# Optimization experiments

Measured on AMD Instinct MI355X. Metric: run time of the kernel, lower is better.

Reference implementation:

```python
import jax, jax.numpy as jnp
import numpy as np

EPS = 1e-6
N_HEADS = 128
QK_NOPE = 128
QK_ROPE = 64
KV_RANK = 512

def rmsnorm(x, gamma):
    var = jnp.mean(jnp.square(x), axis=-1, keepdims=True)
    return x * jax.lax.rsqrt(var + EPS) * gamma

def apply_rope(x, cos, sin):
    # x: [..., D], cos/sin broadcastable to x; rotate-half convention
    x1, x2 = jnp.split(x, 2, axis=-1)
    rot = jnp.concatenate([-x2, x1], axis=-1)
    return x * cos + rot * sin

def setup_inputs() -> dict:
    key = jax.random.key(0)
    ks = jax.random.split(key, 6)
    T, H = 4096, 7168
    inp = {
        "token_x": jax.random.normal(ks[0], (T, H), jnp.float32),
        "wq_a": jax.random.normal(ks[1], (H, 1536), jnp.float32) * 0.02,
        "wq_b": jax.random.normal(ks[2], (1536, N_HEADS * (QK_NOPE + QK_ROPE)), jnp.float32) * 0.02,
        "wkv": jax.random.normal(ks[3], (H, KV_RANK + QK_ROPE), jnp.float32) * 0.02,
        "rope_cos": jax.random.uniform(ks[4], (T, QK_ROPE), jnp.float32, -1.0, 1.0),
        "rope_sin": jax.random.uniform(ks[5], (T, QK_ROPE), jnp.float32, -1.0, 1.0),
        "gamma_cq": jnp.ones((1536,), jnp.float32),
        "gamma_ckv": jnp.ones((KV_RANK,), jnp.float32),
    }
    return inp

def reference(token_x, wq_a, wq_b, wkv, rope_cos, rope_sin, gamma_cq, gamma_ckv):
    T = token_x.shape[0]
    # Query path: down-proj -> RMSNorm -> up-proj -> split -> RoPE on rope part
    cq = rmsnorm(token_x @ wq_a, gamma_cq)                    # [T, 1536]
    q = (cq @ wq_b).reshape(T, N_HEADS, QK_NOPE + QK_ROPE)    # [T, H, 192]
    q_nope, q_rope = q[..., :QK_NOPE], q[..., QK_NOPE:]
    q_rope = apply_rope(q_rope, rope_cos[:, None, :], rope_sin[:, None, :])
    query = jnp.concatenate([q_nope, q_rope], axis=-1)        # [T, H, 192]
    # KV path: joint down-proj -> split latent / rope-key -> RMSNorm + RoPE
    kv = token_x @ wkv                                        # [T, 576]
    ckv = rmsnorm(kv[:, :KV_RANK], gamma_ckv)                 # [T, 512]
    k_rope = apply_rope(kv[:, KV_RANK:], rope_cos, rope_sin)  # [T, 64]
    # Pack outputs into a single array: [T, H*192 + 512 + 64]
    return jnp.concatenate([query.reshape(T, -1), ckv, k_rope], axis=-1)
```

## Files before the change

### kernel.cpp

```cpp
#include <hip/hip_runtime.h>


typedef __attribute__((ext_vector_type(8))) __bf16 bf16x8;
typedef __attribute__((ext_vector_type(4))) float f32x4;

#define OUT_LD 25152

__device__ __forceinline__ unsigned short f2bf(float f) {
  union { float f; unsigned u; } v; v.f = f;
  unsigned r = v.u + 0x7FFFu + ((v.u >> 16) & 1u);
  return (unsigned short)(r >> 16);
}

__device__ __forceinline__ void gload16(const void* g, void* l) {
  __builtin_amdgcn_global_load_lds(
      (__attribute__((address_space(1))) void*)(void*)g,
      (__attribute__((address_space(3))) void*)l, 16, 0, 0);
}

__global__ void cvt_bf16(const float* __restrict__ in, unsigned short* __restrict__ out) {
  size_t i = (size_t)blockIdx.x * 256 + threadIdx.x;
  float4 f = ((const float4*)in)[i];
  ushort4 o;
  o.x = f2bf(f.x); o.y = f2bf(f.y); o.z = f2bf(f.z); o.w = f2bf(f.w);
  ((ushort4*)out)[i] = o;
}

__global__ void transpose_cvt(const float* __restrict__ in, unsigned short* __restrict__ out,
                              int K, int N, int Npad) {
  __shared__ float tile[32][33];
  int k0 = blockIdx.x * 32, n0 = blockIdx.y * 32;
  int tx = threadIdx.x, ty = threadIdx.y;
#pragma unroll
  for (int i = 0; i < 4; ++i) {
    int k = k0 + ty + i * 8;
    int n = n0 + tx;
    tile[ty + i * 8][tx] = (n < N) ? in[(size_t)k * N + n] : 0.f;
  }
  __syncthreads();
#pragma unroll
  for (int i = 0; i < 4; ++i) {
    int n = n0 + ty + i * 8;
    int k = k0 + tx;
    if (n < Npad) out[(size_t)n * K + k] = f2bf(tile[tx][ty + i * 8]);
  }
}

__global__ __launch_bounds__(512, 2) void gemm256(
    const unsigned short* __restrict__ A, const unsigned short* __restrict__ B,
    float* __restrict__ C, int K, int ldc, int Mtiles,
    const float* __restrict__ cs, const float* __restrict__ sn, int rope) {
  __shared__ __attribute__((aligned(128))) char lds[131072];
  const int tid = threadIdx.x;
  const int lane = tid & 63;
  const int wr = (tid >> 6) >> 2;
  const int wc = (tid >> 6) & 3;
  const int NT = K >> 6;

  const int nwg = gridDim.x;
  const int per = nwg >> 3;
  const int bid = blockIdx.x;
  const int swz = (bid & 7) * per + (bid >> 3);
  const int bm = swz % Mtiles, bn = swz / Mtiles;

  const int strow = tid >> 3;
  const int stcolb = (((tid & 7) ^ ((tid >> 3) & 7)) << 4);
  const size_t abase = (size_t)(bm * 256) * K;
  const size_t bbase = (size_t)(bn * 256) * K;

  f32x4 acc[2][2][4][2];
  const f32x4 z4 = {0.f, 0.f, 0.f, 0.f};
#pragma unroll
  for (int a = 0; a < 2; ++a)
#pragma unroll
    for (int b = 0; b < 2; ++b)
#pragma unroll
      for (int c = 0; c < 4; ++c)
#pragma unroll
        for (int d = 0; d < 2; ++d) acc[a][b][c][d] = z4;

#define STAGE_A(kt, bsel, u)                                                          \
  do {                                                                                \
    int row_ = (u) * 64 + strow;                                                      \
    gload16((const char*)(A + abase + (size_t)row_ * K + (size_t)(kt) * 64) + stcolb, \
            lds + (bsel) * 65536 + (u) * 8192 + tid * 16);                            \
  } while (0)
#define STAGE_B(kt, bsel, u)                                                          \
  do {                                                                                \
    int lrow_ = (u) * 64 + strow;                                                     \
    int n_ = ((lrow_ >> 5) & 3) * 64 + ((lrow_ >> 7) & 1) * 32 + (lrow_ & 31);        \
    gload16((const char*)(B + bbase + (size_t)n_ * K + (size_t)(kt) * 64) + stcolb,   \
            lds + (bsel) * 65536 + 32768 + (u) * 8192 + tid * 16);                    \
  } while (0)

  STAGE_A(0, 0, 0); STAGE_A(0, 0, 1); STAGE_A(0, 0, 2); STAGE_A(0, 0, 3);
  STAGE_B(0, 0, 0); STAGE_B(0, 0, 1); STAGE_B(0, 0, 2); STAGE_B(0, 0, 3);
  if (NT > 1) {
    STAGE_A(1, 1, 0); STAGE_A(1, 1, 1);
    STAGE_B(1, 1, 2); STAGE_B(1, 1, 3);
    asm volatile("s_waitcnt vmcnt(4)" ::: "memory");
  } else {
    asm volatile("s_waitcnt vmcnt(0)" ::: "memory");
  }
  __builtin_amdgcn_s_barrier();
  __builtin_amdgcn_sched_barrier(0);

#define PHASE(QM, QN, STAGES)                                                         \
  do {                                                                                \
    const char* Lb_ = lds + buf * 65536;                                              \
    bf16x8 af_[4][2], bb_[2][2];                                                      \
    _Pragma("unroll") for (int mf = 0; mf < 4; ++mf)                                  \
        _Pragma("unroll") for (int ks = 0; ks < 2; ++ks) {                            \
      int row_ = (QM) * 128 + wr * 64 + mf * 16 + (lane & 15);                        \
      int in_ = (ks * 64 + ((lane >> 4) << 4)) ^ ((row_ & 7) << 4);                   \
      af_[mf][ks] = *(const bf16x8*)(Lb_ + row_ * 128 + in_);                         \
    }                                                                                 \
    _Pragma("unroll") for (int nf = 0; nf < 2; ++nf)                                  \
        _Pragma("unroll") for (int ks = 0; ks < 2; ++ks) {                            \
      int c_ = wc * 64 + (QN) * 32 + nf * 16 + (lane & 15);                           \
      int rr_ = ((c_ >> 5) & 1) * 128 + ((c_ >> 6) & 3) * 32 + (c_ & 31);             \
      int in_ = (ks * 64 + ((lane >> 4) << 4)) ^ ((rr_ & 7) << 4);                    \
      bb_[nf][ks] = *(const bf16x8*)(Lb_ + 32768 + rr_ * 128 + in_);                  \
    }                                                                                 \
    STAGES;                                                                           \
    __builtin_amdgcn_s_barrier();                                                     \
    asm volatile("s_waitcnt lgkmcnt(0)" ::: "memory");                                \
    __builtin_amdgcn_sched_barrier(0);                                                \
    __builtin_amdgcn_s_setprio(1);                                                    \
    _Pragma("unroll") for (int mf = 0; mf < 4; ++mf)                                  \
        _Pragma("unroll") for (int nf = 0; nf < 2; ++nf)                              \
            _Pragma("unroll") for (int ks = 0; ks < 2; ++ks)                          \
                acc[QM][QN][mf][nf] = __builtin_amdgcn_mfma_f32_16x16x32_bf16(        \
                    af_[mf][ks], bb_[nf][ks], acc[QM][QN][mf][nf], 0, 0, 0);          \
    __builtin_amdgcn_s_setprio(0);                                                    \
  } while (0)

  for (int t = 0; t < NT; ++t) {
    const int buf = t & 1;
    const int pb = buf ^ 1;
    PHASE(0, 0, { if (t + 1 < NT) { STAGE_A(t + 1, pb, 2); STAGE_A(t + 1, pb, 3); } });
    __builtin_amdgcn_s_barrier();
    PHASE(0, 1, { if (t + 1 < NT) { STAGE_B(t + 1, pb, 0); STAGE_B(t + 1, pb, 1); } });
    __builtin_amdgcn_s_barrier();
    PHASE(1, 1, { if (t + 2 < NT) { STAGE_A(t + 2, buf, 0); STAGE_A(t + 2, buf, 1); } });
    __builtin_amdgcn_s_barrier();
    PHASE(1, 0, { if (t + 2 < NT) { STAGE_B(t + 2, buf, 2); STAGE_B(t + 2, buf, 3); } });
    if (t + 2 < NT) {
      asm volatile("s_waitcnt vmcnt(4)" ::: "memory");
    } else {
      asm volatile("s_waitcnt vmcnt(0)" ::: "memory");
    }
    __builtin_amdgcn_s_barrier();
    __builtin_amdgcn_sched_barrier(0);
  }

  const int colbase = bn * 256 + wc * 64;
  const int rbase = bm * 256 + wr * 64 + ((lane >> 4) << 2);
  const bool isrope = rope && ((colbase % 192) == 128);
  if (isrope) {
#pragma unroll
    for (int qm = 0; qm < 2; ++qm)
#pragma unroll
      for (int mf = 0; mf < 4; ++mf)
#pragma unroll
        for (int nf = 0; nf < 2; ++nf) {
          int i_ = nf * 16 + (lane & 15);
#pragma unroll
          for (int r = 0; r < 4; ++r) {
            int trow = rbase + qm * 128 + mf * 16 + r;
            float c1 = cs[trow * 64 + i_], s1 = sn[trow * 64 + i_];
            float c2 = cs[trow * 64 + 32 + i_], s2 = sn[trow * 64 + 32 + i_];
            float a = acc[qm][0][mf][nf][r], b = acc[qm][1][mf][nf][r];
            C[(size_t)trow * ldc + colbase + i_] = a * c1 - b * s1;
            C[(size_t)trow * ldc + colbase + 32 + i_] = b * c2 + a * s2;
          }
        }
  } else {
#pragma unroll
    for (int qm = 0; qm < 2; ++qm)
#pragma unroll
      for (int qn = 0; qn < 2; ++qn)
#pragma unroll
        for (int mf = 0; mf < 4; ++mf)
#pragma unroll
          for (int nf = 0; nf < 2; ++nf)
#pragma unroll
            for (int r = 0; r < 4; ++r) {
              int trow = rbase + qm * 128 + mf * 16 + r;
              C[(size_t)trow * ldc + colbase + qn * 32 + nf * 16 + (lane & 15)] =
                  acc[qm][qn][mf][nf][r];
            }
  }
#undef PHASE
#undef STAGE_A
#undef STAGE_B
}

__global__ __launch_bounds__(256, 2) void gemm128(
    const unsigned short* __restrict__ A, const unsigned short* __restrict__ B,
    float* __restrict__ C, int K, int ldc, int Nvalid) {
  __shared__ __attribute__((aligned(128))) unsigned short As[128 * 32];
  __shared__ __attribute__((aligned(128))) unsigned short Bs[128 * 32];
  const int tid = threadIdx.x;
  const int lane = tid & 63;
  const int wid = tid >> 6;
  const int wr = wid >> 1, wc = wid & 1;
  const int bm = blockIdx.y, bn = blockIdx.x;
  const size_t abase = (size_t)bm * 128 * K;
  const size_t bbase = (size_t)bn * 128 * K;

  f32x4 acc[4][4];
  const f32x4 zero4 = {0.f, 0.f, 0.f, 0.f};
#pragma unroll
  for (int m = 0; m < 4; ++m)
#pragma unroll
    for (int n = 0; n < 4; ++n) acc[m][n] = zero4;

  const int r0 = tid >> 2;
  const int c0 = (tid & 3) * 8;

  for (int k0 = 0; k0 < K; k0 += 32) {
    gload16(A + abase + (size_t)r0 * K + k0 + c0, As + tid * 8);
    gload16(A + abase + (size_t)(r0 + 64) * K + k0 + c0, As + (256 + tid) * 8);
    gload16(B + bbase + (size_t)r0 * K + k0 + c0, Bs + tid * 8);
    gload16(B + bbase + (size_t)(r0 + 64) * K + k0 + c0, Bs + (256 + tid) * 8);
    __syncthreads();
    bf16x8 af[4], bfr[4];
#pragma unroll
    for (int m = 0; m < 4; ++m)
      af[m] = *(const bf16x8*)(As + (wr * 64 + m * 16 + (lane & 15)) * 32 + (lane >> 4) * 8);
#pragma unroll
    for (int n = 0; n < 4; ++n)
      bfr[n] = *(const bf16x8*)(Bs + (wc * 64 + n * 16 + (lane & 15)) * 32 + (lane >> 4) * 8);
#pragma unroll
    for (int m = 0; m < 4; ++m)
#pragma unroll
      for (int n = 0; n < 4; ++n)
        acc[m][n] = __builtin_amdgcn_mfma_f32_16x16x32_bf16(af[m], bfr[n], acc[m][n], 0, 0, 0);
    __syncthreads();
  }

  const int crow0 = bm * 128 + wr * 64 + ((lane >> 4) << 2);
  const int ccol0 = bn * 128 + wc * 64 + (lane & 15);
#pragma unroll
  for (int m = 0; m < 4; ++m) {
#pragma unroll
    for (int n = 0; n < 4; ++n) {
      int col = ccol0 + n * 16;
      if (col < Nvalid) {
#pragma unroll
        for (int r = 0; r < 4; ++r) {
          int row = crow0 + m * 16 + r;
          C[(size_t)row * ldc + col] = acc[m][n][r];
        }
      }
    }
  }
}

__global__ void rmsnorm_cq(const float* __restrict__ raw, const float* __restrict__ gamma,
                           unsigned short* __restrict__ out) {
  __shared__ float red[4];
  int t = blockIdx.x, tid = threadIdx.x;
  const float* r = raw + (size_t)t * 2176;
  float v[6];
  float ss = 0.f;
#pragma unroll
  for (int i = 0; i < 6; ++i) {
    v[i] = r[tid + i * 256];
    ss += v[i] * v[i];
  }
#pragma unroll
  for (int o = 32; o > 0; o >>= 1) ss += __shfl_xor(ss, o, 64);
  if ((tid & 63) == 0) red[tid >> 6] = ss;
  __syncthreads();
  ss = red[0] + red[1] + red[2] + red[3];
  float sc = rsqrtf(ss * (1.f / 1536.f) + 1e-6f);
#pragma unroll
  for (int i = 0; i < 6; ++i)
    out[(size_t)t * 1536 + tid + i * 256] = f2bf(v[i] * sc * gamma[tid + i * 256]);
}

__global__ void kv_epi(const float* __restrict__ raw, const float* __restrict__ gamma,
                       const float* __restrict__ cs, const float* __restrict__ sn,
                       float* __restrict__ out) {
  __shared__ float red[4];
  int t = blockIdx.x, tid = threadIdx.x;
  const float* r = raw + (size_t)t * 2176 + 1536;
  float v0 = r[tid], v1 = r[tid + 256];
  float ss = v0 * v0 + v1 * v1;
#pragma unroll
  for (int o = 32; o > 0; o >>= 1) ss += __shfl_xor(ss, o, 64);
  if ((tid & 63) == 0) red[tid >> 6] = ss;
  __syncthreads();
  ss = red[0] + red[1] + red[2] + red[3];
  float sc = rsqrtf(ss * (1.f / 512.f) + 1e-6f);
  float* orow = out + (size_t)t * OUT_LD + 24576;
  orow[tid] = v0 * sc * gamma[tid];
  orow[tid + 256] = v1 * sc * gamma[tid + 256];
  if (tid < 32) {
    float a = r[512 + tid], b = r[544 + tid];
    orow[512 + tid] = a * cs[t * 64 + tid] - b * sn[t * 64 + tid];
    orow[544 + tid] = b * cs[t * 64 + 32 + tid] + a * sn[t * 64 + 32 + tid];
  }
}

extern "C" void kernel_launch(void* const* d_in, const int* in_sizes, int n_in,
                              void* d_out, int out_size, void* d_ws, size_t ws_size,
                              hipStream_t stream) {
  const float* token_x = (const float*)d_in[0];
  const float* wq_a = (const float*)d_in[1];
  const float* wq_b = (const float*)d_in[2];
  const float* wkv = (const float*)d_in[3];
  const float* rope_cos = (const float*)d_in[4];
  const float* rope_sin = (const float*)d_in[5];
  const float* gamma_cq = (const float*)d_in[6];
  const float* gamma_ckv = (const float*)d_in[7];
  float* out = (float*)d_out;

  char* ws = (char*)d_ws;
  unsigned short* txb = (unsigned short*)ws;
  unsigned short* wqbT = (unsigned short*)(ws + 58720256);
  unsigned short* Bc = (unsigned short*)(ws + 134217728);
  float* raw = (float*)(ws + 165412864);
  unsigned short* cqb = (unsigned short*)(ws + 201064448);

  cvt_bf16<<<28672, 256, 0, stream>>>(token_x, txb);
  transpose_cvt<<<dim3(7168 / 32, 1536 / 32), dim3(32, 8), 0, stream>>>(wq_a, Bc, 7168, 1536, 1536);
  transpose_cvt<<<dim3(7168 / 32, 640 / 32), dim3(32, 8), 0, stream>>>(
      wkv, Bc + (size_t)1536 * 7168, 7168, 576, 640);
  transpose_cvt<<<dim3(1536 / 32, 24576 / 32), dim3(32, 8), 0, stream>>>(wq_b, wqbT, 1536, 24576, 24576);

  gemm128<<<dim3(17, 32), 256, 0, stream>>>(txb, Bc, raw, 7168, 2176, 2176);

  rmsnorm_cq<<<4096, 256, 0, stream>>>(raw, gamma_cq, cqb);
  kv_epi<<<4096, 256, 0, stream>>>(raw, gamma_ckv, rope_cos, rope_sin, out);

  gemm256<<<1536, 512, 0, stream>>>(cqb, wqbT, out, 1536, OUT_LD, 16, rope_cos, rope_sin, 1);
}
```

Before: 732.4 us.

## Reuse LDS fragments across quadrant MFMAs instead of reloading per phase

The main GEMM loop used to reload A and B fragments from LDS for each of the four output quadrants. It now loads two A fragment sets and two B fragment sets once per k-tile and reuses them across the quadrants in the order (0,0),(0,1),(1,1),(1,0). LDS reads are overlapped with MFMAs using partial lgkmcnt waits. This halves LDS read traffic per tile but holds more fragments live in registers, which could raise register pressure under the 2-wave occupancy bound.

```diff
diff --git a/kernel.cpp b/kernel.cpp
--- a/kernel.cpp
+++ b/kernel.cpp
@@ -93,6 +93,36 @@
             lds + (bsel) * 65536 + 32768 + (u) * 8192 + tid * 16);                    \
   } while (0)
 
+#define READ_A(dst, QM)                                                     \
+  do {                                                                      \
+    _Pragma("unroll") for (int mf = 0; mf < 4; ++mf)                        \
+        _Pragma("unroll") for (int ks = 0; ks < 2; ++ks) {                  \
+      int row_ = (QM) * 128 + wr * 64 + mf * 16 + (lane & 15);              \
+      int in_ = (ks * 64 + ((lane >> 4) << 4)) ^ ((row_ & 7) << 4);         \
+      dst[mf][ks] = *(const bf16x8*)(Lb + row_ * 128 + in_);                \
+    }                                                                       \
+  } while (0)
+#define READ_B(dst, QN)                                                     \
+  do {                                                                      \
+    _Pragma("unroll") for (int nf = 0; nf < 2; ++nf)                        \
+        _Pragma("unroll") for (int ks = 0; ks < 2; ++ks) {                  \
+      int c_ = wc * 64 + (QN) * 32 + nf * 16 + (lane & 15);                 \
+      int rr_ = ((c_ >> 5) & 1) * 128 + ((c_ >> 6) & 3) * 32 + (c_ & 31);   \
+      int in_ = (ks * 64 + ((lane >> 4) << 4)) ^ ((rr_ & 7) << 4);          \
+      dst[nf][ks] = *(const bf16x8*)(Lb + 32768 + rr_ * 128 + in_);         \
+    }                                                                       \
+  } while (0)
+#define MFMA_Q(QM, QN, AF, BB)                                              \
+  do {                                                                      \
+    __builtin_amdgcn_s_setprio(1);                                          \
+    _Pragma("unroll") for (int mf = 0; mf < 4; ++mf)                        \
+        _Pragma("unroll") for (int nf = 0; nf < 2; ++nf)                    \
+            _Pragma("unroll") for (int ks = 0; ks < 2; ++ks)                \
+                acc[QM][QN][mf][nf] = __builtin_amdgcn_mfma_f32_16x16x32_bf16( \
+                    AF[mf][ks], BB[nf][ks], acc[QM][QN][mf][nf], 0, 0, 0);  \
+    __builtin_amdgcn_s_setprio(0);                                          \
+  } while (0)
+
   STAGE_A(0, 0, 0); STAGE_A(0, 0, 1); STAGE_A(0, 0, 2); STAGE_A(0, 0, 3);
   STAGE_B(0, 0, 0); STAGE_B(0, 0, 1); STAGE_B(0, 0, 2); STAGE_B(0, 0, 3);
   if (NT > 1) {
@@ -105,46 +135,43 @@
   __builtin_amdgcn_s_barrier();
   __builtin_amdgcn_sched_barrier(0);
 
-#define PHASE(QM, QN, STAGES)                                                         \
-  do {                                                                                \
-    const char* Lb_ = lds + buf * 65536;                                              \
-    bf16x8 af_[4][2], bb_[2][2];                                                      \
-    _Pragma("unroll") for (int mf = 0; mf < 4; ++mf)                                  \
-        _Pragma("unroll") for (int ks = 0; ks < 2; ++ks) {                            \
-      int row_ = (QM) * 128 + wr * 64 + mf * 16 + (lane & 15);                        \
-      int in_ = (ks * 64 + ((lane >> 4) << 4)) ^ ((row_ & 7) << 4);                   \
-      af_[mf][ks] = *(const bf16x8*)(Lb_ + row_ * 128 + in_);                         \
-    }                                                                                 \
-    _Pragma("unroll") for (int nf = 0; nf < 2; ++nf)                                  \
-        _Pragma("unroll") for (int ks = 0; ks < 2; ++ks) {                            \
-      int c_ = wc * 64 + (QN) * 32 + nf * 16 + (lane & 15);                           \
-      int rr_ = ((c_ >> 5) & 1) * 128 + ((c_ >> 6) & 3) * 32 + (c_ & 31);             \
-      int in_ = (ks * 64 + ((lane >> 4) << 4)) ^ ((rr_ & 7) << 4);                    \
-      bb_[nf][ks] = *(const bf16x8*)(Lb_ + 32768 + rr_ * 128 + in_);                  \
-    }                                                                                 \
-    STAGES;                                                                           \
-    __builtin_amdgcn_s_barrier();                                                     \
-    asm volatile("s_waitcnt lgkmcnt(0)" ::: "memory");                                \
-    __builtin_amdgcn_sched_barrier(0);                                                \
-    __builtin_amdgcn_s_setprio(1);                                                    \
-    _Pragma("unroll") for (int mf = 0; mf < 4; ++mf)                                  \
-        _Pragma("unroll") for (int nf = 0; nf < 2; ++nf)                              \
-            _Pragma("unroll") for (int ks = 0; ks < 2; ++ks)                          \
-                acc[QM][QN][mf][nf] = __builtin_amdgcn_mfma_f32_16x16x32_bf16(        \
-                    af_[mf][ks], bb_[nf][ks], acc[QM][QN][mf][nf], 0, 0, 0);          \
-    __builtin_amdgcn_s_setprio(0);                                                    \
-  } while (0)
-
   for (int t = 0; t < NT; ++t) {
     const int buf = t & 1;
     const int pb = buf ^ 1;
-    PHASE(0, 0, { if (t + 1 < NT) { STAGE_A(t + 1, pb, 2); STAGE_A(t + 1, pb, 3); } });
-    __builtin_amdgcn_s_barrier();
-    PHASE(0, 1, { if (t + 1 < NT) { STAGE_B(t + 1, pb, 0); STAGE_B(t + 1, pb, 1); } });
-    __builtin_amdgcn_s_barrier();
-    PHASE(1, 1, { if (t + 2 < NT) { STAGE_A(t + 2, buf, 0); STAGE_A(t + 2, buf, 1); } });
-    __builtin_amdgcn_s_barrier();
-    PHASE(1, 0, { if (t + 2 < NT) { STAGE_B(t + 2, buf, 2); STAGE_B(t + 2, buf, 3); } });
+    const char* Lb = lds + buf * 65536;
+    bf16x8 af0[4][2], af1[4][2], bb0[2][2], bb1[2][2];
+
+    READ_A(af0, 0);
+    READ_B(bb0, 0);
+    __builtin_amdgcn_sched_barrier(0);
+    READ_B(bb1, 1);
+
+    if (t + 1 < NT) { STAGE_A(t + 1, pb, 2); STAGE_A(t + 1, pb, 3); }
+    __builtin_amdgcn_s_barrier();
+    asm volatile("s_waitcnt lgkmcnt(4)" ::: "memory");
+    __builtin_amdgcn_sched_barrier(0);
+    MFMA_Q(0, 0, af0, bb0);
+    __builtin_amdgcn_s_barrier();
+
+    if (t + 1 < NT) { STAGE_B(t + 1, pb, 0); STAGE_B(t + 1, pb, 1); }
+    __builtin_amdgcn_s_barrier();
+    asm volatile("s_waitcnt lgkmcnt(0)" ::: "memory");
+    __builtin_amdgcn_sched_barrier(0);
+    READ_A(af1, 1);
+    MFMA_Q(0, 1, af0, bb1);
+    __builtin_amdgcn_s_barrier();
+
+    if (t + 2 < NT) { STAGE_A(t + 2, buf, 0); STAGE_A(t + 2, buf, 1); }
+    __builtin_amdgcn_s_barrier();
+    asm volatile("s_waitcnt lgkmcnt(0)" ::: "memory");
+    __builtin_amdgcn_sched_barrier(0);
+    MFMA_Q(1, 1, af1, bb1);
+    __builtin_amdgcn_s_barrier();
+
+    if (t + 2 < NT) { STAGE_B(t + 2, buf, 2); STAGE_B(t + 2, buf, 3); }
+    __builtin_amdgcn_s_barrier();
+    MFMA_Q(1, 0, af1, bb0);
+
     if (t + 2 < NT) {
       asm volatile("s_waitcnt vmcnt(4)" ::: "memory");
     } else {
@@ -191,9 +218,11 @@
                   acc[qm][qn][mf][nf][r];
             }
   }
-#undef PHASE
+#undef MFMA_Q
+#undef READ_B
+#undef READ_A
+#undef STAGE_B
 #undef STAGE_A
-#undef STAGE_B
 }
 
 __global__ __launch_bounds__(256, 2) void gemm128(
```

Result: faster. 699.8 us (-4.5%).
